# Kernel tuning notes

Hardware: AMD Instinct MI355X
Metric: run time of the kernel (lower is better)

## Reference

```python
import jax, jax.numpy as jnp
import numpy as np
import math

NUM_HEADS = 12


def _rope_tables(nph, npw, half_head_dim):
    # grid coords: x = column index, y = row index, flattened row-major
    rows = jnp.arange(nph, dtype=jnp.float32)
    cols = jnp.arange(npw, dtype=jnp.float32)
    gy, gx = jnp.meshgrid(rows, cols, indexing='ij')
    coords = jnp.stack([gx.ravel(), gy.ravel()], axis=1)  # [N, 2]
    cmin = coords.min(axis=0, keepdims=True)
    cmax = coords.max(axis=0, keepdims=True)
    nc = (coords - cmin) / (cmax - cmin + 1e-8)
    div = jnp.exp(jnp.arange(0, half_head_dim, 2, dtype=jnp.float32)
                  * (-(math.log(10000.0) / half_head_dim)))  # [half/2]
    px = nc[:, 0:1] * div  # [N, half/2]
    py = nc[:, 1:2] * div
    rep = lambda t: jnp.repeat(t, 2, axis=-1)  # interleave: even/odd slots get same value
    return rep(jnp.cos(px)), rep(jnp.sin(px)), rep(jnp.cos(py)), rep(jnp.sin(py))


def _apply_rope(t, cos_x, sin_x, cos_y, sin_y):
    # t: [B, H, N, Dh]; tables: [N, Dh//2] broadcast over B, H
    half = t.shape[-1] // 2
    tx, ty = t[..., :half], t[..., half:]
    rx = tx * cos_x + jnp.roll(tx, 1, axis=-1) * sin_x
    ry = ty * cos_y + jnp.roll(ty, 1, axis=-1) * sin_y
    return jnp.concatenate([rx, ry], axis=-1)


def setup_inputs() -> dict:
    key = jax.random.key(0)
    k1, k2, k3 = jax.random.split(key, 3)
    B, S, E = 32, 577, 768  # 24*24 patches + 1 CLS token
    x = jax.random.normal(k1, (B, S, E), dtype=jnp.float32)
    w_qkv = jax.random.normal(k2, (3 * E, E), dtype=jnp.float32) * 0.02
    w_proj = jax.random.normal(k3, (E, E), dtype=jnp.float32) * 0.02
    return {"x": x, "w_qkv": w_qkv, "w_proj": w_proj,
            "num_patches_h": 24, "num_patches_w": 24}


def reference(x, w_qkv, w_proj, num_patches_h, num_patches_w):
    B, S, E = x.shape
    H = NUM_HEADS
    Dh = E // H
    # QKV projection (bias=False)
    qkv = jnp.einsum('bse,fe->bsf', x, w_qkv).reshape(B, S, 3, H, Dh)
    qkv = jnp.transpose(qkv, (2, 0, 3, 1, 4))  # [3, B, H, S, Dh]
    q, k, v = qkv[0], qkv[1], qkv[2]
    # 2D RoPE on patch tokens only (CLS at position 0 unchanged)
    cx, sx, cy, sy = _rope_tables(num_patches_h, num_patches_w, Dh // 2)
    q_patch = _apply_rope(q[:, :, 1:], cx, sx, cy, sy)
    k_patch = _apply_rope(k[:, :, 1:], cx, sx, cy, sy)
    q = jnp.concatenate([q[:, :, :1], q_patch], axis=2)
    k = jnp.concatenate([k[:, :, :1], k_patch], axis=2)
    # scaled dot-product attention (standard backend, dropout=0)
    attn = jnp.einsum('bhqd,bhkd->bhqk', q, k) * (Dh ** -0.5)
    attn = jax.nn.softmax(attn, axis=-1)
    out = jnp.einsum('bhqk,bhkd->bhqd', attn, v)
    out = jnp.transpose(out, (0, 2, 1, 3)).reshape(B, S, E)
    return out @ w_proj.T
```

## Files before the change

### kernel.cpp

```cpp
#include <hip/hip_runtime.h>
#include <hip/hip_bf16.h>
#include <cstdint>


typedef __attribute__((ext_vector_type(8))) short bf16x8;
typedef __attribute__((ext_vector_type(4))) float f32x4;

#define MFMA16(a, b, c) __builtin_amdgcn_mfma_f32_16x16x32_bf16((a), (b), (c), 0, 0, 0)

#define S_LEN 577
#define NHEAD 12
#define DHEAD 64
#define EMB   768
#define F3    2304

__device__ __forceinline__ void gload_lds16(const __hip_bfloat16* g, __hip_bfloat16* l) {
    __builtin_amdgcn_global_load_lds(
        (const __attribute__((address_space(1))) unsigned int*)g,
        (__attribute__((address_space(3))) unsigned int*)l, 16, 0, 0);
}

__device__ __forceinline__ uint4 load8_f32(const float* p) {
    const float4 f0 = *(const float4*)p;
    const float4 f1 = *(const float4*)(p + 4);
    union { uint4 u; __hip_bfloat16 h[8]; } r;
    r.h[0] = __float2bfloat16(f0.x); r.h[1] = __float2bfloat16(f0.y);
    r.h[2] = __float2bfloat16(f0.z); r.h[3] = __float2bfloat16(f0.w);
    r.h[4] = __float2bfloat16(f1.x); r.h[5] = __float2bfloat16(f1.y);
    r.h[6] = __float2bfloat16(f1.z); r.h[7] = __float2bfloat16(f1.w);
    return r.u;
}

__global__ __launch_bounds__(256) void cvt_f32_bf16(
    const float* __restrict__ src, __hip_bfloat16* __restrict__ dst, int n8)
{
    const int i = blockIdx.x * 256 + threadIdx.x;
    if (i < n8)
        *(uint4*)(dst + (size_t)i * 8) = load8_f32(src + (size_t)i * 8);
}

template<bool BF32, bool CF32>
__global__ __launch_bounds__(256) void gemm_a_dma(
    const __hip_bfloat16* __restrict__ A, int lda,
    const void* __restrict__ Bv, int ldb,
    void* __restrict__ Cv, int M, int N, int K)
{
    __shared__ __hip_bfloat16 As[128 * 32];
    __shared__ __hip_bfloat16 Bs[128 * 32];

    const int t      = threadIdx.x;
    const int l      = t & 63;
    const int w      = t >> 6;
    const int lane15 = l & 15;
    const int quad   = l >> 4;

    const int n0 = blockIdx.x * 128;
    const int m0 = blockIdx.y * 128;
    const int wm = (w >> 1) * 64;
    const int wn = (w & 1) * 64;

    const int srow   = t >> 2;
    const int schunk = t & 3;

    int ar0 = m0 + srow;       if (ar0 > M - 1) ar0 = M - 1;
    int ar1 = m0 + 64 + srow;  if (ar1 > M - 1) ar1 = M - 1;
    const int br0 = n0 + srow;
    const int br1 = n0 + 64 + srow;

    const __hip_bfloat16* pa0 = A + (size_t)ar0 * lda + schunk * 8;
    const __hip_bfloat16* pa1 = A + (size_t)ar1 * lda + schunk * 8;
    const size_t b0off = (size_t)br0 * ldb + schunk * 8;
    const size_t b1off = (size_t)br1 * ldb + schunk * 8;

    __hip_bfloat16* lAs0 = As + srow * 32 + schunk * 8;
    __hip_bfloat16* lAs1 = As + (64 + srow) * 32 + schunk * 8;
    __hip_bfloat16* lBs0 = Bs + srow * 32 + schunk * 8;
    __hip_bfloat16* lBs1 = Bs + (64 + srow) * 32 + schunk * 8;

    f32x4 acc[4][4] = {};

    for (int k0 = 0; k0 < K; k0 += 32) {
        uint4 vb0, vb1;
        if constexpr (BF32) {
            vb0 = load8_f32((const float*)Bv + b0off + k0);
            vb1 = load8_f32((const float*)Bv + b1off + k0);
        }
        __syncthreads();
        gload_lds16(pa0 + k0, lAs0);
        gload_lds16(pa1 + k0, lAs1);
        if constexpr (BF32) {
            *(uint4*)lBs0 = vb0;
            *(uint4*)lBs1 = vb1;
        } else {
            gload_lds16((const __hip_bfloat16*)Bv + b0off + k0, lBs0);
            gload_lds16((const __hip_bfloat16*)Bv + b1off + k0, lBs1);
        }
        __syncthreads();

        bf16x8 a[4], b[4];
        #pragma unroll
        for (int i = 0; i < 4; ++i)
            a[i] = *(const bf16x8*)(As + (wm + i * 16 + lane15) * 32 + quad * 8);
        #pragma unroll
        for (int j = 0; j < 4; ++j)
            b[j] = *(const bf16x8*)(Bs + (wn + j * 16 + lane15) * 32 + quad * 8);

        #pragma unroll
        for (int i = 0; i < 4; ++i)
            #pragma unroll
            for (int j = 0; j < 4; ++j)
                acc[i][j] = MFMA16(a[i], b[j], acc[i][j]);
    }

    #pragma unroll
    for (int i = 0; i < 4; ++i) {
        #pragma unroll
        for (int r = 0; r < 4; ++r) {
            const int m = m0 + wm + i * 16 + quad * 4 + r;
            if (m < M) {
                #pragma unroll
                for (int j = 0; j < 4; ++j) {
                    const int n = n0 + wn + j * 16 + lane15;
                    if constexpr (CF32)
                        ((float*)Cv)[(size_t)m * N + n] = acc[i][j][r];
                    else
                        ((__hip_bfloat16*)Cv)[(size_t)m * N + n] = __float2bfloat16(acc[i][j][r]);
                }
            }
        }
    }
}

__global__ __launch_bounds__(256) void rope_kernel(__hip_bfloat16* __restrict__ qkv)
{
    const int p = blockIdx.x;
    const int b = blockIdx.y;
    const int l = threadIdx.x & 63;
    const int w = threadIdx.x >> 6;

    const int jj   = l & 31;
    const float i2 = (float)((jj >> 1) * 2);
    const float dv = __expf(-i2 * 0.28782313662425576f);
    const float inv = 1.0f / (23.0f + 1e-8f);
    const float cx = (float)(p % 24) * inv;
    const float cy = (float)(p / 24) * inv;
    const float ang = ((l < 32) ? cx : cy) * dv;
    const float c = __cosf(ang);
    const float s = __sinf(ang);
    const int nb = (l & 32) | ((jj + 31) & 31);

    const size_t rowbase = ((size_t)(b * S_LEN + 1 + p)) * F3;

    for (int pr = w; pr < 24; pr += 4) {
        const int part = pr / 12;
        const int h    = pr % 12;
        const size_t off = rowbase + (size_t)part * EMB + h * DHEAD + l;
        float v  = __bfloat162float(qkv[off]);
        float vp = __shfl(v, nb, 64);
        qkv[off] = __float2bfloat16(v * c + vp * s);
    }
}

__global__ __launch_bounds__(512) void attn_kernel(
    const __hip_bfloat16* __restrict__ qkv,
    __hip_bfloat16* __restrict__ attn_out, int ldo)
{
    __shared__ __hip_bfloat16 Qs[128][72];
    __shared__ __hip_bfloat16 Ks[64][72];
    __shared__ __hip_bfloat16 Vt[64][72];

    const int t      = threadIdx.x;
    const int l      = t & 63;
    const int w      = t >> 6;
    const int lane15 = l & 15;
    const int quad   = l >> 4;

    const int q0 = blockIdx.x * 128;
    const int h  = blockIdx.y;
    const int b  = blockIdx.z;

    {
        const int row = t >> 2, seg = t & 3;
        int gq = q0 + row; if (gq > S_LEN - 1) gq = S_LEN - 1;
        const uint4* src = (const uint4*)(qkv + (size_t)(b * S_LEN + gq) * F3 + h * DHEAD + seg * 16);
        uint4 u0 = src[0], u1 = src[1];
        const __hip_bfloat16* e0 = (const __hip_bfloat16*)&u0;
        const __hip_bfloat16* e1 = (const __hip_bfloat16*)&u1;
        #pragma unroll
        for (int i = 0; i < 8; ++i) {
            Qs[row][seg * 16 + i]     = __float2bfloat16(__bfloat162float(e0[i]) * 0.125f);
            Qs[row][seg * 16 + 8 + i] = __float2bfloat16(__bfloat162float(e1[i]) * 0.125f);
        }
    }
    __syncthreads();

    bf16x8 qf0 = *(const bf16x8*)&Qs[w * 16 + lane15][quad * 8];
    bf16x8 qf1 = *(const bf16x8*)&Qs[w * 16 + lane15][32 + quad * 8];

    f32x4 o[4] = {};
    float m_i[4] = {-3.0e38f, -3.0e38f, -3.0e38f, -3.0e38f};
    float l_i[4] = {0.f, 0.f, 0.f, 0.f};

    for (int s0 = 0; s0 < S_LEN; s0 += 64) {
        __syncthreads();
        {
            const int row = t >> 3, seg8 = t & 7;
            int gk = s0 + row; if (gk > S_LEN - 1) gk = S_LEN - 1;
            const uint4* src = (const uint4*)(qkv + (size_t)(b * S_LEN + gk) * F3 + EMB + h * DHEAD);
            *(uint4*)&Ks[row][seg8 * 8] = src[seg8];
        }
        {
            const int s = t & 63, dg = t >> 6;
            int gk = s0 + s; if (gk > S_LEN - 1) gk = S_LEN - 1;
            const uint4* src = (const uint4*)(qkv + (size_t)(b * S_LEN + gk) * F3 + 2 * EMB + h * DHEAD);
            uint4 u0 = src[dg];
            const __hip_bfloat16* e0 = (const __hip_bfloat16*)&u0;
            #pragma unroll
            for (int i = 0; i < 8; ++i)
                Vt[dg * 8 + i][s] = e0[i];
        }
        __syncthreads();

        f32x4 sf[4];
        #pragma unroll
        for (int nt = 0; nt < 4; ++nt) {
            f32x4 z = {0.f, 0.f, 0.f, 0.f};
            bf16x8 k0f = *(const bf16x8*)&Ks[nt * 16 + lane15][quad * 8];
            bf16x8 k1f = *(const bf16x8*)&Ks[nt * 16 + lane15][32 + quad * 8];
            z = MFMA16(qf0, k0f, z);
            z = MFMA16(qf1, k1f, z);
            sf[nt] = z;
        }
        #pragma unroll
        for (int nt = 0; nt < 4; ++nt) {
            if (s0 + nt * 16 + lane15 >= S_LEN)
                sf[nt] = (f32x4){-1e30f, -1e30f, -1e30f, -1e30f};
        }

        float alpha[4];
        #pragma unroll
        for (int r = 0; r < 4; ++r) {
            float mx = fmaxf(fmaxf(sf[0][r], sf[1][r]), fmaxf(sf[2][r], sf[3][r]));
            #pragma unroll
            for (int off = 1; off < 16; off <<= 1)
                mx = fmaxf(mx, __shfl_xor(mx, off, 64));
            float mnew = fmaxf(m_i[r], mx);
            alpha[r] = __expf(m_i[r] - mnew);
            m_i[r] = mnew;
        }

        float pv[4][4];
        #pragma unroll
        for (int nt = 0; nt < 4; ++nt)
            #pragma unroll
            for (int r = 0; r < 4; ++r)
                pv[nt][r] = __expf(sf[nt][r] - m_i[r]);

        #pragma unroll
        for (int r = 0; r < 4; ++r) {
            float sum = pv[0][r] + pv[1][r] + pv[2][r] + pv[3][r];
            #pragma unroll
            for (int off = 1; off < 16; off <<= 1)
                sum += __shfl_xor(sum, off, 64);
            l_i[r] = l_i[r] * alpha[r] + sum;
        }

        #pragma unroll
        for (int ci = 0; ci < 4; ++ci)
            #pragma unroll
            for (int r = 0; r < 4; ++r)
                o[ci][r] *= alpha[r];

        #pragma unroll
        for (int nt = 0; nt < 4; ++nt)
            #pragma unroll
            for (int r = 0; r < 4; ++r)
                Qs[w * 16 + quad * 4 + r][nt * 16 + lane15] = __float2bfloat16(pv[nt][r]);
        asm volatile("s_waitcnt lgkmcnt(0)" ::: "memory");

        #pragma unroll
        for (int s32 = 0; s32 < 2; ++s32) {
            bf16x8 pa = *(const bf16x8*)&Qs[w * 16 + lane15][s32 * 32 + quad * 8];
            #pragma unroll
            for (int ci = 0; ci < 4; ++ci) {
                bf16x8 vb = *(const bf16x8*)&Vt[ci * 16 + lane15][s32 * 32 + quad * 8];
                o[ci] = MFMA16(pa, vb, o[ci]);
            }
        }
    }

    #pragma unroll
    for (int r = 0; r < 4; ++r) {
        const int q = q0 + w * 16 + quad * 4 + r;
        if (q < S_LEN) {
            const float rl = 1.0f / l_i[r];
            #pragma unroll
            for (int ci = 0; ci < 4; ++ci) {
                attn_out[(size_t)(b * S_LEN + q) * ldo + h * DHEAD + ci * 16 + lane15] =
                    __float2bfloat16(o[ci][r] * rl);
            }
        }
    }
}

extern "C" void kernel_launch(void* const* d_in, const int* in_sizes, int n_in,
                              void* d_out, int out_size, void* d_ws, size_t ws_size,
                              hipStream_t stream) {
    const float* x      = (const float*)d_in[0];
    const float* w_qkv  = (const float*)d_in[1];
    const float* w_proj = (const float*)d_in[2];
    for (int i = 0; i < n_in; ++i) {
        if      (in_sizes[i] == 32 * S_LEN * EMB) x      = (const float*)d_in[i];
        else if (in_sizes[i] == F3 * EMB)         w_qkv  = (const float*)d_in[i];
        else if (in_sizes[i] == EMB * EMB)        w_proj = (const float*)d_in[i];
    }
    float* out = (float*)d_out;

    const int Mrows = 32 * S_LEN;
    const int NX    = Mrows * EMB;
    const int NWQ   = F3 * EMB;

    __hip_bfloat16* qkv = (__hip_bfloat16*)d_ws;
    __hip_bfloat16* xb  = (__hip_bfloat16*)d_out;
    __hip_bfloat16* wb  = xb + (size_t)NX;

    cvt_f32_bf16<<<NX / 8 / 256, 256, 0, stream>>>(x, xb, NX / 8);
    cvt_f32_bf16<<<NWQ / 8 / 256, 256, 0, stream>>>(w_qkv, wb, NWQ / 8);
    gemm_a_dma<false, false><<<dim3(F3 / 128, (Mrows + 127) / 128), 256, 0, stream>>>(
        xb, EMB, wb, EMB, qkv, Mrows, F3, EMB);
    rope_kernel<<<dim3(576, 32), 256, 0, stream>>>(qkv);
    attn_kernel<<<dim3((S_LEN + 127) / 128, NHEAD, 32), 512, 0, stream>>>(qkv, qkv, F3);
    gemm_a_dma<true, true><<<dim3(EMB / 128, (Mrows + 127) / 128), 256, 0, stream>>>(
        qkv, F3, w_proj, EMB, out, Mrows, EMB, EMB);
}
```

Baseline: 416.7 us.

## Prefetch next K/V tile into registers and transpose QK^T MFMA for lane-local softmax

```diff
diff --git a/kernel.cpp b/kernel.cpp
--- a/kernel.cpp
+++ b/kernel.cpp
@@ -13,6 +13,7 @@
 #define DHEAD 64
 #define EMB   768
 #define F3    2304
+#define NT_KV 10
 
 __device__ __forceinline__ void gload_lds16(const __hip_bfloat16* g, __hip_bfloat16* l) {
     __builtin_amdgcn_global_load_lds(
@@ -179,6 +180,17 @@
     const int h  = blockIdx.y;
     const int b  = blockIdx.z;
 
+    const int krow = t >> 3, kseg = t & 7;
+    const int vs   = t & 63, vdg = t >> 6;
+
+    uint4 ku, vu;
+    {
+        int gk = krow; if (gk > S_LEN - 1) gk = S_LEN - 1;
+        ku = ((const uint4*)(qkv + (size_t)(b * S_LEN + gk) * F3 + EMB + h * DHEAD))[kseg];
+        int gv = vs;  if (gv > S_LEN - 1) gv = S_LEN - 1;
+        vu = ((const uint4*)(qkv + (size_t)(b * S_LEN + gv) * F3 + 2 * EMB + h * DHEAD))[vdg];
+    }
+
     {
         const int row = t >> 2, seg = t & 3;
         int gq = q0 + row; if (gq > S_LEN - 1) gq = S_LEN - 1;
@@ -198,28 +210,27 @@
     bf16x8 qf1 = *(const bf16x8*)&Qs[w * 16 + lane15][32 + quad * 8];
 
     f32x4 o[4] = {};
-    float m_i[4] = {-3.0e38f, -3.0e38f, -3.0e38f, -3.0e38f};
-    float l_i[4] = {0.f, 0.f, 0.f, 0.f};
-
-    for (int s0 = 0; s0 < S_LEN; s0 += 64) {
+    float m_i = -3.0e38f;
+    float l_i = 0.f;
+
+    for (int ti = 0; ti < NT_KV; ++ti) {
         __syncthreads();
+        *(uint4*)&Ks[krow][kseg * 8] = ku;
         {
-            const int row = t >> 3, seg8 = t & 7;
-            int gk = s0 + row; if (gk > S_LEN - 1) gk = S_LEN - 1;
-            const uint4* src = (const uint4*)(qkv + (size_t)(b * S_LEN + gk) * F3 + EMB + h * DHEAD);
-            *(uint4*)&Ks[row][seg8 * 8] = src[seg8];
-        }
-        {
-            const int s = t & 63, dg = t >> 6;
-            int gk = s0 + s; if (gk > S_LEN - 1) gk = S_LEN - 1;
-            const uint4* src = (const uint4*)(qkv + (size_t)(b * S_LEN + gk) * F3 + 2 * EMB + h * DHEAD);
-            uint4 u0 = src[dg];
-            const __hip_bfloat16* e0 = (const __hip_bfloat16*)&u0;
+            const __hip_bfloat16* e0 = (const __hip_bfloat16*)&vu;
             #pragma unroll
             for (int i = 0; i < 8; ++i)
-                Vt[dg * 8 + i][s] = e0[i];
-        }
-        __syncthreads();
+                Vt[vdg * 8 + i][vs] = e0[i];
+        }
+        if (ti + 1 < NT_KV) {
+            int gk = (ti + 1) * 64 + krow; if (gk > S_LEN - 1) gk = S_LEN - 1;
+            ku = ((const uint4*)(qkv + (size_t)(b * S_LEN + gk) * F3 + EMB + h * DHEAD))[kseg];
+            int gv = (ti + 1) * 64 + vs;  if (gv > S_LEN - 1) gv = S_LEN - 1;
+            vu = ((const uint4*)(qkv + (size_t)(b * S_LEN + gv) * F3 + 2 * EMB + h * DHEAD))[vdg];
+        }
+        asm volatile("s_waitcnt lgkmcnt(0)" ::: "memory");
+        __builtin_amdgcn_s_barrier();
+        asm volatile("" ::: "memory");
 
         f32x4 sf[4];
         #pragma unroll
@@ -227,55 +238,56 @@
             f32x4 z = {0.f, 0.f, 0.f, 0.f};
             bf16x8 k0f = *(const bf16x8*)&Ks[nt * 16 + lane15][quad * 8];
             bf16x8 k1f = *(const bf16x8*)&Ks[nt * 16 + lane15][32 + quad * 8];
-            z = MFMA16(qf0, k0f, z);
-            z = MFMA16(qf1, k1f, z);
+            z = MFMA16(k0f, qf0, z);
+            z = MFMA16(k1f, qf1, z);
             sf[nt] = z;
         }
+        const int s0 = ti * 64;
+        #pragma unroll
+        for (int nt = 0; nt < 4; ++nt)
+            #pragma unroll
+            for (int r = 0; r < 4; ++r)
+                if (s0 + nt * 16 + quad * 4 + r >= S_LEN) sf[nt][r] = -1e30f;
+
+        float mx = fmaxf(fmaxf(sf[0][0], sf[0][1]), fmaxf(sf[0][2], sf[0][3]));
+        #pragma unroll
+        for (int nt = 1; nt < 4; ++nt)
+            mx = fmaxf(mx, fmaxf(fmaxf(sf[nt][0], sf[nt][1]), fmaxf(sf[nt][2], sf[nt][3])));
+        mx = fmaxf(mx, __shfl_xor(mx, 16, 64));
+        mx = fmaxf(mx, __shfl_xor(mx, 32, 64));
+
+        const float mnew  = fmaxf(m_i, mx);
+        const float alpha = __expf(m_i - mnew);
+        m_i = mnew;
+
+        float sum = 0.f;
         #pragma unroll
         for (int nt = 0; nt < 4; ++nt) {
-            if (s0 + nt * 16 + lane15 >= S_LEN)
-                sf[nt] = (f32x4){-1e30f, -1e30f, -1e30f, -1e30f};
-        }
-
-        float alpha[4];
-        #pragma unroll
-        for (int r = 0; r < 4; ++r) {
-            float mx = fmaxf(fmaxf(sf[0][r], sf[1][r]), fmaxf(sf[2][r], sf[3][r]));
-            #pragma unroll
-            for (int off = 1; off < 16; off <<= 1)
-                mx = fmaxf(mx, __shfl_xor(mx, off, 64));
-            float mnew = fmaxf(m_i[r], mx);
-            alpha[r] = __expf(m_i[r] - mnew);
-            m_i[r] = mnew;
-        }
-
-        float pv[4][4];
+            #pragma unroll
+            for (int r = 0; r < 4; ++r) {
+                sf[nt][r] = __expf(sf[nt][r] - mnew);
+                sum += sf[nt][r];
+            }
+        }
+        sum += __shfl_xor(sum, 16, 64);
+        sum += __shfl_xor(sum, 32, 64);
+        l_i = l_i * alpha + sum;
+
+        float af[4];
+        #pragma unroll
+        for (int r = 0; r < 4; ++r)
+            af[r] = __shfl(alpha, quad * 4 + r, 64);
+        #pragma unroll
+        for (int ci = 0; ci < 4; ++ci)
+            #pragma unroll
+            for (int r = 0; r < 4; ++r)
+                o[ci][r] *= af[r];
+
         #pragma unroll
         for (int nt = 0; nt < 4; ++nt)
             #pragma unroll
             for (int r = 0; r < 4; ++r)
-                pv[nt][r] = __expf(sf[nt][r] - m_i[r]);
-
-        #pragma unroll
-        for (int r = 0; r < 4; ++r) {
-            float sum = pv[0][r] + pv[1][r] + pv[2][r] + pv[3][r];
-            #pragma unroll
-            for (int off = 1; off < 16; off <<= 1)
-                sum += __shfl_xor(sum, off, 64);
-            l_i[r] = l_i[r] * alpha[r] + sum;
-        }
-
-        #pragma unroll
-        for (int ci = 0; ci < 4; ++ci)
-            #pragma unroll
-            for (int r = 0; r < 4; ++r)
-                o[ci][r] *= alpha[r];
-
-        #pragma unroll
-        for (int nt = 0; nt < 4; ++nt)
-            #pragma unroll
-            for (int r = 0; r < 4; ++r)
-                Qs[w * 16 + quad * 4 + r][nt * 16 + lane15] = __float2bfloat16(pv[nt][r]);
+                Qs[w * 16 + lane15][nt * 16 + quad * 4 + r] = __float2bfloat16(sf[nt][r]);
         asm volatile("s_waitcnt lgkmcnt(0)" ::: "memory");
 
         #pragma unroll
@@ -291,9 +303,10 @@
 
     #pragma unroll
     for (int r = 0; r < 4; ++r) {
+        const float lr = __shfl(l_i, quad * 4 + r, 64);
         const int q = q0 + w * 16 + quad * 4 + r;
         if (q < S_LEN) {
-            const float rl = 1.0f / l_i[r];
+            const float rl = 1.0f / lr;
             #pragma unroll
             for (int ci = 0; ci < 4; ++ci) {
                 attn_out[(size_t)(b * S_LEN + q) * ldo + h * DHEAD + ci * 16 + lane15] =
```

Measured after the change: 379.6 us. 1.1x faster.
